# Optimization experiments

Hardware: AMD Instinct MI355X
Metric: run time of the kernel (lower is better)

The kernel has to match this reference:

```python
import jax, jax.numpy as jnp
import numpy as np

N_NODES = 50000


def gcn_conv(x, src, dst, deg_inv_sqrt, W, b, n_nodes):
    # GCNConv: h = x @ W; msg = norm * h[src]; out = scatter_add(msg, dst) + b
    h = x @ W  # [N, out]
    norm = deg_inv_sqrt[src] * deg_inv_sqrt[dst]  # symmetric normalization
    msg = h[src] * norm[:, None]  # [E+N, out]
    out = jax.ops.segment_sum(msg, dst, num_segments=n_nodes)
    return out + b


def setup_inputs() -> dict:
    key = jax.random.key(0)
    k_x, k_e, k_w1, k_w2 = jax.random.split(key, 4)
    in_c, hid, out_c = 256, 64, 64
    x = jax.random.normal(k_x, (N_NODES, 256), dtype=jnp.float32)
    edge_index = jax.random.randint(k_e, (2, 1600000), 0, N_NODES, dtype=jnp.int64)
    # Glorot-ish weights, zero bias as in GCNConv defaults
    W1 = jax.random.normal(k_w1, (in_c, hid), dtype=jnp.float32) / np.sqrt(in_c)
    b1 = jnp.zeros((hid,), dtype=jnp.float32)
    W2 = jax.random.normal(k_w2, (hid, out_c), dtype=jnp.float32) / np.sqrt(hid)
    b2 = jnp.zeros((out_c,), dtype=jnp.float32)
    return {"x": x, "edge_index": edge_index, "W1": W1, "b1": b1, "W2": W2, "b2": b2}


def reference(x, edge_index, W1, b1, W2, b2):
    n = x.shape[0]
    loops = jnp.arange(n, dtype=edge_index.dtype)
    src = jnp.concatenate([edge_index[0], loops])  # add self-loops
    dst = jnp.concatenate([edge_index[1], loops])
    deg = jax.ops.segment_sum(jnp.ones_like(dst, dtype=x.dtype), dst, num_segments=n)
    deg_inv_sqrt = jnp.where(deg > 0, jax.lax.rsqrt(deg), 0.0)
    h = gcn_conv(x, src, dst, deg_inv_sqrt, W1, b1, n)
    h = jax.nn.relu(h)
    out = gcn_conv(h, src, dst, deg_inv_sqrt, W2, b2, n)
    return out
```

## Files before the change

kernel.cpp:

```cpp
#include <hip/hip_runtime.h>
#include <hip/hip_bf16.h>


#define NB_MAX 1024

__device__ inline unsigned short f2bf(float f) {
    unsigned u = __builtin_bit_cast(unsigned, f);
    return (unsigned short)((u + 0x7FFFu + ((u >> 16) & 1u)) >> 16);
}
__device__ inline float bf2f(unsigned short b) {
    return __builtin_bit_cast(float, (unsigned)b << 16);
}


__global__ __launch_bounds__(256) void k_hist(const int* __restrict__ ei, int E,
                                              int nb, int chunk,
                                              int* __restrict__ histT) {
    __shared__ int h[NB_MAX];
    for (int i = threadIdx.x; i < nb; i += 256) h[i] = 0;
    __syncthreads();
    int e0 = blockIdx.x * chunk, e1 = min(E, e0 + chunk);
    for (int e = e0 + threadIdx.x; e < e1; e += 256)
        atomicAdd(&h[ei[E + e] >> 6], 1);
    __syncthreads();
    for (int b = threadIdx.x; b < nb; b += 256)
        histT[b * 256 + blockIdx.x] = h[b];
}


__global__ __launch_bounds__(256) void k_scan_cols(int* __restrict__ histT,
                                                   int* __restrict__ total) {
    __shared__ int sm[256];
    int b = blockIdx.x, t = threadIdx.x;
    int v = histT[b * 256 + t];
    sm[t] = v;
    __syncthreads();
    for (int off = 1; off < 256; off <<= 1) {
        int u = (t >= off) ? sm[t - off] : 0;
        __syncthreads();
        sm[t] += u;
        __syncthreads();
    }
    histT[b * 256 + t] = sm[t] - v;
    if (t == 255) total[b] = sm[255];
}


__global__ __launch_bounds__(1024) void k_scan_totals(const int* __restrict__ total,
                                                      int* __restrict__ base, int nb) {
    __shared__ int sm[1024];
    int t = threadIdx.x;
    int v = (t < nb) ? total[t] : 0;
    sm[t] = v;
    __syncthreads();
    for (int off = 1; off < 1024; off <<= 1) {
        int u = (t >= off) ? sm[t - off] : 0;
        __syncthreads();
        sm[t] += u;
        __syncthreads();
    }
    if (t < nb) base[t] = sm[t] - v;
    if (t == nb - 1) base[nb] = sm[t];
}


__global__ __launch_bounds__(256) void k_scatter(const int* __restrict__ ei, int E,
                                                 int nb, int chunk,
                                                 const int* __restrict__ histT,
                                                 const int* __restrict__ base,
                                                 unsigned* __restrict__ packed) {
    __shared__ int cur[NB_MAX];
    for (int b = threadIdx.x; b < nb; b += 256)
        cur[b] = base[b] + histT[b * 256 + blockIdx.x];
    __syncthreads();
    int e0 = blockIdx.x * chunk, e1 = min(E, e0 + chunk);
    for (int e = e0 + threadIdx.x; e < e1; e += 256) {
        int s = ei[e], d = ei[E + e];
        int pos = atomicAdd(&cur[d >> 6], 1);
        packed[pos] = (unsigned)s | ((unsigned)(d & 63) << 16);
    }
}


__global__ __launch_bounds__(256) void k_csr(const unsigned* __restrict__ packed,
                                             const int* __restrict__ base, int n,
                                             int* __restrict__ offs,
                                             float* __restrict__ dinv,
                                             unsigned short* __restrict__ ssrc) {
    __shared__ int cnt[64];
    __shared__ int cur[64];
    const int b = blockIdx.x, t = threadIdx.x;
    const int p0 = base[b], p1 = base[b + 1];
    if (t < 64) cnt[t] = 0;
    __syncthreads();
    for (int p = p0 + t; p < p1; p += 256)
        atomicAdd(&cnt[(packed[p] >> 16) & 63], 1);
    __syncthreads();
    if (t < 64) {
        int s = cnt[t];
        int sum = s;
#pragma unroll
        for (int d = 1; d < 64; d <<= 1) {
            int u = __shfl_up(sum, d, 64);
            if (t >= d) sum += u;
        }
        int excl = sum - s;
        int node = (b << 6) + t;
        if (node < n) {
            offs[node] = p0 + excl;
            dinv[node] = 1.0f / sqrtf((float)(s + 1));
        }
        cur[t] = p0 + excl;
    }
    if (b == 0 && t == 0) offs[n] = base[(n + 63) >> 6];
    __syncthreads();
    for (int p = p0 + t; p < p1; p += 256) {
        unsigned k = packed[p];
        int pos = atomicAdd(&cur[(k >> 16) & 63], 1);
        ssrc[pos] = (unsigned short)(k & 0xFFFFu);
    }
}


#define FMA4(A, s, wv)                                                         \
    (A).x += (s) * (wv).x; (A).y += (s) * (wv).y;                              \
    (A).z += (s) * (wv).z; (A).w += (s) * (wv).w;

template <int K>
__global__ __launch_bounds__(256) void k_gemm(const float* __restrict__ X,
                                              const float* __restrict__ W,
                                              const float* __restrict__ dinv,
                                              unsigned short* __restrict__ HS,
                                              int n) {
    __shared__ float xl[64][36];
    __shared__ float wl[32][64];

    const int t = threadIdx.x;
    const int tc = t & 15;
    const int tr = t >> 4;
    const int row0 = blockIdx.x * 64;

    float4 acc[4];
    acc[0] = acc[1] = acc[2] = acc[3] = make_float4(0.f, 0.f, 0.f, 0.f);

    for (int k0 = 0; k0 < K; k0 += 32) {
#pragma unroll
        for (int i = 0; i < 2; ++i) {
            int idx = i * 256 + t;
            int r = idx >> 3, f4 = idx & 7;
            int gr = row0 + r;
            float4 v = make_float4(0.f, 0.f, 0.f, 0.f);
            if (gr < n) v = *(const float4*)(X + (size_t)gr * K + k0 + f4 * 4);
            *(float4*)&xl[r][f4 * 4] = v;
        }
#pragma unroll
        for (int i = 0; i < 2; ++i) {
            int idx = i * 256 + t;
            int kr = idx >> 4, f4 = idx & 15;
            *(float4*)&wl[kr][f4 * 4] =
                *(const float4*)(W + (size_t)(k0 + kr) * 64 + f4 * 4);
        }
        __syncthreads();

#pragma unroll
        for (int kk = 0; kk < 32; kk += 4) {
            float4 xv0 = *(float4*)&xl[tr * 4 + 0][kk];
            float4 xv1 = *(float4*)&xl[tr * 4 + 1][kk];
            float4 xv2 = *(float4*)&xl[tr * 4 + 2][kk];
            float4 xv3 = *(float4*)&xl[tr * 4 + 3][kk];
            float4 wv0 = *(float4*)&wl[kk + 0][tc * 4];
            float4 wv1 = *(float4*)&wl[kk + 1][tc * 4];
            float4 wv2 = *(float4*)&wl[kk + 2][tc * 4];
            float4 wv3 = *(float4*)&wl[kk + 3][tc * 4];

            FMA4(acc[0], xv0.x, wv0); FMA4(acc[0], xv0.y, wv1);
            FMA4(acc[0], xv0.z, wv2); FMA4(acc[0], xv0.w, wv3);
            FMA4(acc[1], xv1.x, wv0); FMA4(acc[1], xv1.y, wv1);
            FMA4(acc[1], xv1.z, wv2); FMA4(acc[1], xv1.w, wv3);
            FMA4(acc[2], xv2.x, wv0); FMA4(acc[2], xv2.y, wv1);
            FMA4(acc[2], xv2.z, wv2); FMA4(acc[2], xv2.w, wv3);
            FMA4(acc[3], xv3.x, wv0); FMA4(acc[3], xv3.y, wv1);
            FMA4(acc[3], xv3.z, wv2); FMA4(acc[3], xv3.w, wv3);
        }
        __syncthreads();
    }

#pragma unroll
    for (int ri = 0; ri < 4; ++ri) {
        int gr = row0 + tr * 4 + ri;
        if (gr < n) {
            float dv = dinv[gr];
            float4 o = acc[ri];
            ushort4 pk;
            pk.x = f2bf(o.x * dv); pk.y = f2bf(o.y * dv);
            pk.z = f2bf(o.z * dv); pk.w = f2bf(o.w * dv);
            *(ushort4*)(HS + (size_t)gr * 64 + tc * 4) = pk;
        }
    }
}


template <bool RELU>
__global__ void k_agg(const unsigned short* __restrict__ hs,
                      const int* __restrict__ offs,
                      const unsigned short* __restrict__ ssrc,
                      const float* __restrict__ dinv,
                      const float* __restrict__ bias,
                      float* __restrict__ out, int n, int qmax) {
    int node = blockIdx.x * 4 + (threadIdx.x >> 6);
    if (node >= n) return;
    node = __builtin_amdgcn_readfirstlane(node);
    const int lane = threadIdx.x & 63;
    const int half = lane >> 5;
    const int cp   = lane & 31;

    const unsigned* hsu = (const unsigned*)hs;
    const unsigned* ssu = (const unsigned*)ssrc;

    const int beg = offs[node];
    const int end = offs[node + 1];

    const unsigned sv = hsu[node * 32 + cp];
    const float dv = dinv[node];
    const float2 bv = *(const float2*)(bias + 2 * cp);

    float2 acc = make_float2(0.f, 0.f);
    const int q0 = beg >> 1;
    const int npairs = ((end + 1) >> 1) - q0;

    for (int qb = 0; qb < npairs; qb += 16) {
        unsigned ss[16];
#pragma unroll
        for (int j = 0; j < 16; ++j) {
            int q = q0 + qb + j;
            ss[j] = ssu[q <= qmax ? q : qmax];
        }
        unsigned v[16];
#pragma unroll
        for (int j = 0; j < 16; ++j) {
            int s = half ? (int)(ss[j] >> 16) : (int)(ss[j] & 0xFFFFu);
            v[j] = hsu[s * 32 + cp];
        }
#pragma unroll
        for (int j = 0; j < 16; ++j) {
            int e = 2 * (q0 + qb + j) + half;
            bool live = (e >= beg) & (e < end);
            acc.x += live ? bf2f((unsigned short)(v[j] & 0xFFFFu)) : 0.f;
            acc.y += live ? bf2f((unsigned short)(v[j] >> 16)) : 0.f;
        }
    }

    acc.x += __shfl_xor(acc.x, 32, 64);
    acc.y += __shfl_xor(acc.y, 32, 64);

    float rx = dv * (acc.x + bf2f((unsigned short)(sv & 0xFFFFu))) + bv.x;
    float ry = dv * (acc.y + bf2f((unsigned short)(sv >> 16))) + bv.y;
    if (RELU) { rx = fmaxf(rx, 0.f); ry = fmaxf(ry, 0.f); }
    if (half == 0)
        *(float2*)(out + (size_t)node * 64 + 2 * cp) = make_float2(rx, ry);
}


extern "C" void kernel_launch(void* const* d_in, const int* in_sizes, int n_in,
                              void* d_out, int out_size, void* d_ws, size_t ws_size,
                              hipStream_t stream) {
    const float* x  = (const float*)d_in[0];
    const int*   ei = (const int*)d_in[1];
    const float* W1 = (const float*)d_in[2];
    const float* b1 = (const float*)d_in[3];
    const float* W2 = (const float*)d_in[4];
    const float* b2 = (const float*)d_in[5];

    const int n = in_sizes[0] / 256;
    const int E = in_sizes[1] / 2;
    const int nb = (n + 63) >> 6;
    const int chunk = (E + 255) / 256;
    const int qmax = (E - 2) >> 1;

    char* ws = (char*)d_ws;
    auto carve = [&](size_t bytes) {
        void* p = (void*)ws;
        ws += (bytes + 255) & ~(size_t)255;
        return p;
    };
    int*            histT  = (int*)carve((size_t)nb * 256 * 4);
    int*            total  = (int*)carve((size_t)nb * 4);
    int*            base   = (int*)carve((size_t)(nb + 1) * 4);
    unsigned*       packed = (unsigned*)carve((size_t)E * 4);
    unsigned short* ssrc   = (unsigned short*)carve((size_t)E * 2);
    int*            offs   = (int*)carve((size_t)(n + 1) * 4);
    float*          dinv   = (float*)carve((size_t)n * 4);
    unsigned short* hs1    = (unsigned short*)carve((size_t)n * 64 * 2);
    float*          hB     = (float*)carve((size_t)n * 64 * 4);
    unsigned short* hs2    = (unsigned short*)carve((size_t)n * 64 * 2);

    k_hist<<<256, 256, 0, stream>>>(ei, E, nb, chunk, histT);
    k_scan_cols<<<nb, 256, 0, stream>>>(histT, total);
    k_scan_totals<<<1, 1024, 0, stream>>>(total, base, nb);
    k_scatter<<<256, 256, 0, stream>>>(ei, E, nb, chunk, histT, base, packed);
    k_csr<<<nb, 256, 0, stream>>>(packed, base, n, offs, dinv, ssrc);

    const int nbG = (n + 63) / 64;

    k_gemm<256><<<nbG, 256, 0, stream>>>(x, W1, dinv, hs1, n);
    k_agg<true><<<(n + 3) / 4, 256, 0, stream>>>(hs1, offs, ssrc, dinv, b1, hB,
                                                 n, qmax);

    k_gemm<64><<<nbG, 256, 0, stream>>>(hB, W2, dinv, hs2, n);
    k_agg<false><<<(n + 3) / 4, 256, 0, stream>>>(hs2, offs, ssrc, dinv, b2,
                                                  (float*)d_out, n, qmax);
}
```

Baseline: 240.4 us.

## Pad per-node CSR neighbor lists to even length with dummy zero row

The CSR build now pads each node's neighbor list to an even length and aligns it to a pair boundary. Odd slots are filled with a sentinel index n that points to an all-zero row appended to hs1 and hs2. The aggregation kernel then drops the per-edge liveness masks and qmax clamping: it runs full 16-pair chunks unmasked and handles the remainder by redirecting unused slots to a zero-sentinel pair. The aim is to cut ALU and predicate work in the gather loop, at the cost of a slightly larger index array and extra dummy gathers for odd-degree nodes.

After: 224.3 us. -6.7%, faster.

```diff
diff --git a/kernel.cpp b/kernel.cpp
--- a/kernel.cpp
+++ b/kernel.cpp
@@ -83,10 +83,14 @@
 
 
 __global__ __launch_bounds__(256) void k_csr(const unsigned* __restrict__ packed,
-                                             const int* __restrict__ base, int n,
-                                             int* __restrict__ offs,
+                                             const int* __restrict__ base,
+                                             int n,
+                                             int* __restrict__ qbeg,
+                                             int* __restrict__ qcnt,
                                              float* __restrict__ dinv,
-                                             unsigned short* __restrict__ ssrc) {
+                                             unsigned short* __restrict__ ssrcp,
+                                             unsigned short* __restrict__ hs1,
+                                             unsigned short* __restrict__ hs2) {
     __shared__ int cnt[64];
     __shared__ int cur[64];
     const int b = blockIdx.x, t = threadIdx.x;
@@ -97,27 +101,43 @@
         atomicAdd(&cnt[(packed[p] >> 16) & 63], 1);
     __syncthreads();
     if (t < 64) {
-        int s = cnt[t];
-        int sum = s;
+        int deg = cnt[t];
+        int pdeg = (deg + 1) & ~1;
+        int sum = pdeg;
 #pragma unroll
         for (int d = 1; d < 64; d <<= 1) {
             int u = __shfl_up(sum, d, 64);
             if (t >= d) sum += u;
         }
-        int excl = sum - s;
+        int excl = sum - pdeg;
+        int pb = (2 + p0 + 128 * b + 1) & ~1;
+        int start = pb + excl;
         int node = (b << 6) + t;
         if (node < n) {
-            offs[node] = p0 + excl;
-            dinv[node] = 1.0f / sqrtf((float)(s + 1));
-        }
-        cur[t] = p0 + excl;
-    }
-    if (b == 0 && t == 0) offs[n] = base[(n + 63) >> 6];
+            qbeg[node] = start >> 1;
+            qcnt[node] = pdeg >> 1;
+            dinv[node] = 1.0f / sqrtf((float)(deg + 1));
+        }
+        cur[t] = start;
+    }
     __syncthreads();
     for (int p = p0 + t; p < p1; p += 256) {
         unsigned k = packed[p];
         int pos = atomicAdd(&cur[(k >> 16) & 63], 1);
-        ssrc[pos] = (unsigned short)(k & 0xFFFFu);
+        ssrcp[pos] = (unsigned short)(k & 0xFFFFu);
+    }
+    __syncthreads();
+    if (t < 64 && (cnt[t] & 1))
+        ssrcp[cur[t]] = (unsigned short)n;
+    if (b == 0) {
+        if (t < 64) {
+            hs1[(size_t)n * 64 + t] = 0;
+            hs2[(size_t)n * 64 + t] = 0;
+        }
+        if (t == 0) {
+            ssrcp[0] = (unsigned short)n;
+            ssrcp[1] = (unsigned short)n;
+        }
     }
 }
 
@@ -202,11 +222,12 @@
 
 template <bool RELU>
 __global__ void k_agg(const unsigned short* __restrict__ hs,
-                      const int* __restrict__ offs,
-                      const unsigned short* __restrict__ ssrc,
+                      const int* __restrict__ qbeg,
+                      const int* __restrict__ qcnt,
+                      const unsigned short* __restrict__ ssrcp,
                       const float* __restrict__ dinv,
                       const float* __restrict__ bias,
-                      float* __restrict__ out, int n, int qmax) {
+                      float* __restrict__ out, int n) {
     int node = blockIdx.x * 4 + (threadIdx.x >> 6);
     if (node >= n) return;
     node = __builtin_amdgcn_readfirstlane(node);
@@ -215,26 +236,21 @@
     const int cp   = lane & 31;
 
     const unsigned* hsu = (const unsigned*)hs;
-    const unsigned* ssu = (const unsigned*)ssrc;
-
-    const int beg = offs[node];
-    const int end = offs[node + 1];
+    const unsigned* ssu = (const unsigned*)ssrcp;
+
+    const int q0 = qbeg[node];
+    const int m  = qcnt[node];
 
     const unsigned sv = hsu[node * 32 + cp];
     const float dv = dinv[node];
     const float2 bv = *(const float2*)(bias + 2 * cp);
 
-    float2 acc = make_float2(0.f, 0.f);
-    const int q0 = beg >> 1;
-    const int npairs = ((end + 1) >> 1) - q0;
-
-    for (int qb = 0; qb < npairs; qb += 16) {
+    float ax = 0.f, ay = 0.f;
+    int qb = 0;
+    for (; qb + 16 <= m; qb += 16) {
         unsigned ss[16];
 #pragma unroll
-        for (int j = 0; j < 16; ++j) {
-            int q = q0 + qb + j;
-            ss[j] = ssu[q <= qmax ? q : qmax];
-        }
+        for (int j = 0; j < 16; ++j) ss[j] = ssu[q0 + qb + j];
         unsigned v[16];
 #pragma unroll
         for (int j = 0; j < 16; ++j) {
@@ -243,18 +259,36 @@
         }
 #pragma unroll
         for (int j = 0; j < 16; ++j) {
-            int e = 2 * (q0 + qb + j) + half;
-            bool live = (e >= beg) & (e < end);
-            acc.x += live ? bf2f((unsigned short)(v[j] & 0xFFFFu)) : 0.f;
-            acc.y += live ? bf2f((unsigned short)(v[j] >> 16)) : 0.f;
-        }
-    }
-
-    acc.x += __shfl_xor(acc.x, 32, 64);
-    acc.y += __shfl_xor(acc.y, 32, 64);
-
-    float rx = dv * (acc.x + bf2f((unsigned short)(sv & 0xFFFFu))) + bv.x;
-    float ry = dv * (acc.y + bf2f((unsigned short)(sv >> 16))) + bv.y;
+            ax += __builtin_bit_cast(float, v[j] << 16);
+            ay += __builtin_bit_cast(float, v[j] & 0xFFFF0000u);
+        }
+    }
+    const int rem = m - qb;
+    if (rem) {
+        unsigned ss[16];
+#pragma unroll
+        for (int j = 0; j < 16; ++j) {
+            int q = (j < rem) ? (q0 + qb + j) : 0;
+            ss[j] = ssu[q];
+        }
+        unsigned v[16];
+#pragma unroll
+        for (int j = 0; j < 16; ++j) {
+            int s = half ? (int)(ss[j] >> 16) : (int)(ss[j] & 0xFFFFu);
+            v[j] = hsu[s * 32 + cp];
+        }
+#pragma unroll
+        for (int j = 0; j < 16; ++j) {
+            ax += __builtin_bit_cast(float, v[j] << 16);
+            ay += __builtin_bit_cast(float, v[j] & 0xFFFF0000u);
+        }
+    }
+
+    ax += __shfl_xor(ax, 32, 64);
+    ay += __shfl_xor(ay, 32, 64);
+
+    float rx = dv * (ax + __builtin_bit_cast(float, sv << 16)) + bv.x;
+    float ry = dv * (ay + __builtin_bit_cast(float, sv & 0xFFFF0000u)) + bv.y;
     if (RELU) { rx = fmaxf(rx, 0.f); ry = fmaxf(ry, 0.f); }
     if (half == 0)
         *(float2*)(out + (size_t)node * 64 + 2 * cp) = make_float2(rx, ry);
@@ -275,7 +309,6 @@
     const int E = in_sizes[1] / 2;
     const int nb = (n + 63) >> 6;
     const int chunk = (E + 255) / 256;
-    const int qmax = (E - 2) >> 1;
 
     char* ws = (char*)d_ws;
     auto carve = [&](size_t bytes) {
@@ -287,26 +320,28 @@
     int*            total  = (int*)carve((size_t)nb * 4);
     int*            base   = (int*)carve((size_t)(nb + 1) * 4);
     unsigned*       packed = (unsigned*)carve((size_t)E * 4);
-    unsigned short* ssrc   = (unsigned short*)carve((size_t)E * 2);
-    int*            offs   = (int*)carve((size_t)(n + 1) * 4);
+    unsigned short* ssrcp  = (unsigned short*)carve(((size_t)E + 128 * nb + 256) * 2);
+    int*            qbeg   = (int*)carve((size_t)n * 4);
+    int*            qcnt   = (int*)carve((size_t)n * 4);
     float*          dinv   = (float*)carve((size_t)n * 4);
-    unsigned short* hs1    = (unsigned short*)carve((size_t)n * 64 * 2);
+    unsigned short* hs1    = (unsigned short*)carve((size_t)(n + 1) * 64 * 2);
     float*          hB     = (float*)carve((size_t)n * 64 * 4);
-    unsigned short* hs2    = (unsigned short*)carve((size_t)n * 64 * 2);
+    unsigned short* hs2    = (unsigned short*)carve((size_t)(n + 1) * 64 * 2);
 
     k_hist<<<256, 256, 0, stream>>>(ei, E, nb, chunk, histT);
     k_scan_cols<<<nb, 256, 0, stream>>>(histT, total);
     k_scan_totals<<<1, 1024, 0, stream>>>(total, base, nb);
     k_scatter<<<256, 256, 0, stream>>>(ei, E, nb, chunk, histT, base, packed);
-    k_csr<<<nb, 256, 0, stream>>>(packed, base, n, offs, dinv, ssrc);
+    k_csr<<<nb, 256, 0, stream>>>(packed, base, n, qbeg, qcnt, dinv, ssrcp,
+                                  hs1, hs2);
 
     const int nbG = (n + 63) / 64;
 
     k_gemm<256><<<nbG, 256, 0, stream>>>(x, W1, dinv, hs1, n);
-    k_agg<true><<<(n + 3) / 4, 256, 0, stream>>>(hs1, offs, ssrc, dinv, b1, hB,
-                                                 n, qmax);
+    k_agg<true><<<(n + 3) / 4, 256, 0, stream>>>(hs1, qbeg, qcnt, ssrcp, dinv,
+                                                 b1, hB, n);
 
     k_gemm<64><<<nbG, 256, 0, stream>>>(hB, W2, dinv, hs2, n);
-    k_agg<false><<<(n + 3) / 4, 256, 0, stream>>>(hs2, offs, ssrc, dinv, b2,
-                                                  (float*)d_out, n, qmax);
-}
+    k_agg<false><<<(n + 3) / 4, 256, 0, stream>>>(hs2, qbeg, qcnt, ssrcp, dinv,
+                                                  b2, (float*)d_out, n);
+}
```
